# Kernel optimization log

Hardware: AMD Instinct MI355X
Metric: run time of the kernel (lower is better)

## Reference

```python
import jax, jax.numpy as jnp
import numpy as np

B, T, H, NH, L = 2, 2048, 1024, 16, 6
D = H // NH          # head dim = 64
FF = 4 * H           # MLP hidden = 4096
EPS = 1e-5           # torch LayerNorm default

CAUSAL = np.tril(np.ones((T, T), dtype=bool))  # [T,T] lower-triangular mask


def _ln(x, g, b):
    m = jnp.mean(x, axis=-1, keepdims=True)
    v = jnp.mean(jnp.square(x - m), axis=-1, keepdims=True)
    return (x - m) * jax.lax.rsqrt(v + EPS) * g + b


def _block(x, p):
    Wq, bq, Wk, bk, Wv, bv, Wp, bp, W1, b1, W2, b2, g1, be1, g2, be2 = p
    mask = jnp.asarray(CAUSAL)
    # qkv projections -> [B, NH, T, D]
    q = (x @ Wq + bq).reshape(B, T, NH, D).transpose(0, 2, 1, 3)
    k = (x @ Wk + bk).reshape(B, T, NH, D).transpose(0, 2, 1, 3)
    v = (x @ Wv + bv).reshape(B, T, NH, D).transpose(0, 2, 1, 3)
    scores = jnp.einsum('bhtd,bhsd->bhts', q, k) / jnp.sqrt(jnp.float32(D))
    scores = jnp.where(mask, scores, -jnp.inf)
    attn = jax.nn.softmax(scores, axis=-1)
    o = jnp.einsum('bhts,bhsd->bhtd', attn, v)
    o = o.transpose(0, 2, 1, 3).reshape(B, T, H) @ Wp + bp
    x = _ln(x + o, g1, be1)            # residual then ln1 (post-LN, as in source)
    h = jax.nn.gelu(x @ W1 + b1, approximate=False)
    x = _ln(x + h @ W2 + b2, g2, be2)  # residual then ln2
    return x


def setup_inputs() -> dict:
    key = jax.random.key(0)
    ks = jax.random.split(key, 8)
    s = 0.02
    w = lambda k, shape: jax.random.normal(k, shape, jnp.float32) * s
    return {
        'x':  jax.random.normal(ks[0], (B, T, H), jnp.float32),
        'Wq': w(ks[1], (L, H, H)),  'bq': jnp.zeros((L, H), jnp.float32),
        'Wk': w(ks[2], (L, H, H)),  'bk': jnp.zeros((L, H), jnp.float32),
        'Wv': w(ks[3], (L, H, H)),  'bv': jnp.zeros((L, H), jnp.float32),
        'Wp': w(ks[4], (L, H, H)),  'bp': jnp.zeros((L, H), jnp.float32),
        'W1': w(ks[5], (L, H, FF)), 'b1': jnp.zeros((L, FF), jnp.float32),
        'W2': w(ks[6], (L, FF, H)), 'b2': jnp.zeros((L, H), jnp.float32),
        'g1': jnp.ones((L, H), jnp.float32),  'be1': jnp.zeros((L, H), jnp.float32),
        'g2': jnp.ones((L, H), jnp.float32),  'be2': jnp.zeros((L, H), jnp.float32),
    }


def reference(x, Wq, bq, Wk, bk, Wv, bv, Wp, bp, W1, b1, W2, b2, g1, be1, g2, be2):
    params = (Wq, bq, Wk, bk, Wv, bv, Wp, bp, W1, b1, W2, b2, g1, be1, g2, be2)
    y, _ = jax.lax.scan(lambda c, p: (_block(c, p), None), x, params)
    return y
```

## Files before the change

kernel.cpp:

```cpp
#include <hip/hip_runtime.h>

constexpr int cB  = 2;
constexpr int cT  = 2048;
constexpr int cH  = 1024;
constexpr int cNH = 16;
constexpr int cFF = 4096;
constexpr int cL  = 6;
constexpr int cM  = cB * cT;

typedef __attribute__((ext_vector_type(8))) short short8;
typedef __attribute__((ext_vector_type(4))) float f32x4;
typedef __attribute__((ext_vector_type(4))) unsigned short u16x4;
typedef unsigned short u16;

__device__ __forceinline__ u16 f2bf(float f) {
  union { float f; unsigned int u; } v; v.f = f;
  unsigned int u = v.u;
  return (u16)((u + 0x7fffu + ((u >> 16) & 1u)) >> 16);
}

__device__ __forceinline__ void glds16(const void* g, void* l) {
  __builtin_amdgcn_global_load_lds(
      (__attribute__((address_space(1))) void*)(unsigned long long)g,
      (__attribute__((address_space(3))) void*)(unsigned int)(unsigned long long)l,
      16, 0, 0);
}

#define EPI_F32 0
#define EPI_GELU 1
#define EPI_QKV 2

template <int EPI>
__global__ __launch_bounds__(256) void gemm_bt(
    const u16* __restrict__ A,
    const u16* __restrict__ B0, const u16* __restrict__ B1, const u16* __restrict__ B2,
    const float* __restrict__ bias0, const float* __restrict__ bias1, const float* __restrict__ bias2,
    void* __restrict__ out0, void* __restrict__ out1, void* __restrict__ out2, void* __restrict__ out3,
    int M, int N, int K, int ntn)
{
  __shared__ u16 As[128 * 32];
  __shared__ u16 Bs[128 * 32];
  const int tid = threadIdx.x;
  const int wave = tid >> 6;
  const int lane = tid & 63;
  const int l15 = lane & 15;
  const int q4 = lane >> 4;
  const int mt = blockIdx.x;
  const int by = blockIdx.y;
  const int mat = by / ntn;
  const int nt = by - mat * ntn;
  const u16* BT = (mat == 0) ? B0 : ((mat == 1) ? B1 : B2);
  const float* bias = (mat == 0) ? bias0 : ((mat == 1) ? bias1 : bias2);
  void* out = (mat == 0) ? out0 : ((mat == 1) ? out1 : out2);

  const int kz = blockIdx.z;
  const int kpc = K / gridDim.z;
  const int kb0 = kz * kpc, kb1 = kb0 + kpc;
  if (EPI == EPI_F32) {
    void* outs[4] = {out0, out1, out2, out3};
    out = outs[kz];
    if (kz > 0) bias = nullptr;
  }

  const int wr = (wave >> 1) << 6;
  const int wc = (wave & 1) << 6;

  f32x4 acc[4][4] = {};

  const int srow = (wave << 5) + (lane >> 2);
  const int scol = (lane & 3) << 3;
  const u16* Ag = A + (size_t)(mt * 128 + srow) * K + scol;
  const u16* Bg = BT + (size_t)(nt * 128 + srow) * K + scol;
  u16* AsD = As + (wave << 10);
  u16* BsD = Bs + (wave << 10);

  for (int k0 = kb0; k0 < kb1; k0 += 32) {
    glds16(Ag + k0, AsD);
    glds16(Ag + k0 + 16 * K, AsD + 512);
    glds16(Bg + k0, BsD);
    glds16(Bg + k0 + 16 * K, BsD + 512);
    __syncthreads();
    short8 av[4], bv[4];
#pragma unroll
    for (int i = 0; i < 4; ++i)
      av[i] = *(const short8*)(As + ((wr + i * 16 + l15) << 5) + (q4 << 3));
#pragma unroll
    for (int j = 0; j < 4; ++j)
      bv[j] = *(const short8*)(Bs + ((wc + j * 16 + l15) << 5) + (q4 << 3));
#pragma unroll
    for (int i = 0; i < 4; ++i)
#pragma unroll
      for (int j = 0; j < 4; ++j)
        acc[i][j] = __builtin_amdgcn_mfma_f32_16x16x32_bf16(av[i], bv[j], acc[i][j], 0, 0, 0);
    __syncthreads();
  }

  float bj[4];
#pragma unroll
  for (int j = 0; j < 4; ++j) bj[j] = bias ? bias[nt * 128 + wc + j * 16 + l15] : 0.0f;

  const float qscale = (EPI == EPI_QKV && mat == 0) ? 0.125f : 1.0f;

#pragma unroll
  for (int i = 0; i < 4; ++i) {
#pragma unroll
    for (int j = 0; j < 4; ++j) {
      const int n = nt * 128 + wc + j * 16 + l15;
#pragma unroll
      for (int r = 0; r < 4; ++r) {
        const int m = mt * 128 + wr + i * 16 + (q4 << 2) + r;
        float vv = acc[i][j][r] + bj[j];
        if (EPI == EPI_F32) {
          ((float*)out)[(size_t)m * N + n] = vv;
        } else if (EPI == EPI_GELU) {
          float gg = vv * 0.5f * (1.0f + erff(vv * 0.70710678118654752f));
          ((u16*)out)[(size_t)m * N + n] = f2bf(gg);
        } else {
          const int b = m >> 11, t = m & (cT - 1);
          const int h = n >> 6, d = n & 63;
          ((u16*)out)[((((size_t)b * cNH + h) * cT + t) << 6) + d] = f2bf(vv * qscale);
        }
      }
    }
  }
}

__global__ __launch_bounds__(256) void flash_attn(
    const u16* __restrict__ q, const u16* __restrict__ k,
    const u16* __restrict__ v, u16* __restrict__ o)
{
  __shared__ u16 Vt[2][64 * 80];
  __shared__ u16 Pl[8][16 * 80];

  const int tid = threadIdx.x, wave = tid >> 6, lane = tid & 63;
  const int l15 = lane & 15, q4 = lane >> 4;
  const int bx = blockIdx.x;
  const int qtH = 31 - bx;
  const int qtL = bx;
  const int bh = blockIdx.y;
  const u16* qh = q + ((size_t)bh * cT << 6);
  const u16* kh = k + ((size_t)bh * cT << 6);
  const u16* vh = v + ((size_t)bh * cT << 6);

  short8 qfH[2], qfL[2];
#pragma unroll
  for (int kk = 0; kk < 2; ++kk) {
    qfH[kk] = *(const short8*)(qh + (size_t)((qtH << 6) + wave * 16 + l15) * 64 + kk * 32 + q4 * 8);
    qfL[kk] = *(const short8*)(qh + (size_t)((qtL << 6) + wave * 16 + l15) * 64 + kk * 32 + q4 * 8);
  }

  short8 ones;
#pragma unroll
  for (int i = 0; i < 8; ++i) ones[i] = (short)0x3F80;

  uint4 vs0, vs1;
  auto vload = [&](int st) {
    const int s0 = st << 6;
    const u16* src = vh + (size_t)(s0 + lane) * 64 + wave * 8;
    vs0 = *(const uint4*)(src);
    vs1 = *(const uint4*)(src + 32);
  };
  auto vwrite = [&](int buf) {
    u16* Vb = &Vt[buf][0];
    const int s = lane;
#pragma unroll
    for (int rd = 0; rd < 2; ++rd) {
      const int d0 = wave * 8 + rd * 32;
      uint4 vv = rd ? vs1 : vs0;
      Vb[(d0 + 0) * 80 + s] = (u16)(vv.x & 0xffff);
      Vb[(d0 + 1) * 80 + s] = (u16)(vv.x >> 16);
      Vb[(d0 + 2) * 80 + s] = (u16)(vv.y & 0xffff);
      Vb[(d0 + 3) * 80 + s] = (u16)(vv.y >> 16);
      Vb[(d0 + 4) * 80 + s] = (u16)(vv.z & 0xffff);
      Vb[(d0 + 5) * 80 + s] = (u16)(vv.z >> 16);
      Vb[(d0 + 6) * 80 + s] = (u16)(vv.w & 0xffff);
      Vb[(d0 + 7) * 80 + s] = (u16)(vv.w >> 16);
    }
  };

  auto loadK = [&](int st, short8* kf) {
    const int s0 = st << 6;
#pragma unroll
    for (int j = 0; j < 4; ++j)
#pragma unroll
      for (int kk = 0; kk < 2; ++kk)
        kf[j * 2 + kk] = *(const short8*)(kh + (size_t)(s0 + j * 16 + l15) * 64 + kk * 32 + q4 * 8);
  };

  f32x4 oaH[4] = {}, oaL[4] = {};
  f32x4 lsH = {}, lsL = {};

  auto tileQ = [&](int kt, int qt, const short8* qf, const short8* kf,
                   f32x4* oa, f32x4& ls, int buf, u16* pl) {
    f32x4 sa[4];
#pragma unroll
    for (int j = 0; j < 4; ++j) {
      f32x4 zz = {};
      zz = __builtin_amdgcn_mfma_f32_16x16x32_bf16(qf[0], kf[j * 2 + 0], zz, 0, 0, 0);
      zz = __builtin_amdgcn_mfma_f32_16x16x32_bf16(qf[1], kf[j * 2 + 1], zz, 0, 0, 0);
      sa[j] = zz;
    }
    if (kt == qt) {
#pragma unroll
      for (int r = 0; r < 4; ++r) {
        const int trow = wave * 16 + q4 * 4 + r;
#pragma unroll
        for (int j = 0; j < 4; ++j) {
          float pv = (j * 16 + l15 > trow) ? 0.0f : __expf(sa[j][r]);
          pl[(q4 * 4 + r) * 80 + j * 16 + l15] = f2bf(pv);
        }
      }
    } else {
#pragma unroll
      for (int r = 0; r < 4; ++r)
#pragma unroll
        for (int j = 0; j < 4; ++j)
          pl[(q4 * 4 + r) * 80 + j * 16 + l15] = f2bf(__expf(sa[j][r]));
    }
#pragma unroll
    for (int kk = 0; kk < 2; ++kk) {
      short8 pf = *(const short8*)(&pl[l15 * 80 + kk * 32 + q4 * 8]);
      ls = __builtin_amdgcn_mfma_f32_16x16x32_bf16(pf, ones, ls, 0, 0, 0);
#pragma unroll
      for (int jd = 0; jd < 4; ++jd) {
        short8 vf = *(const short8*)(&Vt[buf][(jd * 16 + l15) * 80 + kk * 32 + q4 * 8]);
        oa[jd] = __builtin_amdgcn_mfma_f32_16x16x32_bf16(pf, vf, oa[jd], 0, 0, 0);
      }
    }
  };

  auto tile = [&](int kt, const short8* kf, int buf) {
    tileQ(kt, qtH, qfH, kf, oaH, lsH, buf, &Pl[wave][0]);
    if (kt <= qtL)
      tileQ(kt, qtL, qfL, kf, oaL, lsL, buf, &Pl[wave + 4][0]);
  };

  const int nk = qtH + 1;
  short8 kfA[8], kfB[8];
  vload(0);
  loadK(0, kfA);
  vwrite(0);
  __syncthreads();

  int kt = 0;
  for (; kt + 2 <= nk; kt += 2) {
    vload(kt + 1);
    loadK(kt + 1, kfB);
    tile(kt, kfA, 0);
    vwrite(1);
    __syncthreads();
    if (kt + 2 < nk) { vload(kt + 2); loadK(kt + 2, kfA); }
    tile(kt + 1, kfB, 1);
    if (kt + 2 < nk) vwrite(0);
    __syncthreads();
  }
  if (kt < nk) { tile(kt, kfA, 0); }

  const int b = bh >> 4, h = bh & 15;
#pragma unroll
  for (int r = 0; r < 4; ++r) {
    const int tH = (qtH << 6) + wave * 16 + (q4 << 2) + r;
    const int tL = (qtL << 6) + wave * 16 + (q4 << 2) + r;
    const float invH = 1.0f / lsH[r];
    const float invL = 1.0f / lsL[r];
#pragma unroll
    for (int jd = 0; jd < 4; ++jd) {
      const int d = jd * 16 + l15;
      o[((size_t)(b * cT + tH)) * cH + (h << 6) + d] = f2bf(oaH[jd][r] * invH);
      o[((size_t)(b * cT + tL)) * cH + (h << 6) + d] = f2bf(oaL[jd][r] * invL);
    }
  }
}

template <int NY>
__global__ __launch_bounds__(256) void add_ln_k(
    const float* __restrict__ x,
    const float* __restrict__ y0, const float* __restrict__ y1,
    const float* __restrict__ y2, const float* __restrict__ y3,
    const float* __restrict__ g, const float* __restrict__ be,
    float* __restrict__ xout, u16* __restrict__ xb)
{
  const float* ys[4] = {y0, y1, y2, y3};
  const int row = blockIdx.x;
  const int c = threadIdx.x << 2;
  const size_t base = ((size_t)row << 10) + c;
  f32x4 vv = *(const f32x4*)(x + base);
#pragma unroll
  for (int p = 0; p < NY; ++p) {
    f32x4 yv = *(const f32x4*)(ys[p] + base);
#pragma unroll
    for (int t = 0; t < 4; ++t) vv[t] += yv[t];
  }
  float s1 = vv[0] + vv[1] + vv[2] + vv[3];
  float s2 = vv[0] * vv[0] + vv[1] * vv[1] + vv[2] * vv[2] + vv[3] * vv[3];
#pragma unroll
  for (int off = 1; off < 64; off <<= 1) {
    s1 += __shfl_xor(s1, off);
    s2 += __shfl_xor(s2, off);
  }
  __shared__ float sm[8];
  const int wave = threadIdx.x >> 6, lane = threadIdx.x & 63;
  if (lane == 0) { sm[wave] = s1; sm[wave + 4] = s2; }
  __syncthreads();
  const float S1 = sm[0] + sm[1] + sm[2] + sm[3];
  const float S2 = sm[4] + sm[5] + sm[6] + sm[7];
  const float mean = S1 * (1.0f / cH);
  const float var = S2 * (1.0f / cH) - mean * mean;
  const float rstd = rsqrtf(var + 1e-5f);
  f32x4 gv = *(const f32x4*)(g + c);
  f32x4 bv = *(const f32x4*)(be + c);
  f32x4 ov; u16x4 ob;
#pragma unroll
  for (int t = 0; t < 4; ++t) {
    ov[t] = (vv[t] - mean) * rstd * gv[t] + bv[t];
    ob[t] = f2bf(ov[t]);
  }
  *(f32x4*)(xout + base) = ov;
  *(u16x4*)(xb + base) = ob;
}

__global__ __launch_bounds__(256) void cvt_bf16(const float* __restrict__ in, u16* __restrict__ out)
{
  const size_t i = ((size_t)blockIdx.x * 256 + threadIdx.x) << 2;
  f32x4 vv = *(const f32x4*)(in + i);
  u16x4 ob;
#pragma unroll
  for (int t = 0; t < 4; ++t) ob[t] = f2bf(vv[t]);
  *(u16x4*)(out + i) = ob;
}

struct TransArgs {
  const float* src[6];
  u16* dst[6];
  int Kd[6];
  int Nd[6];
  int tofs[7];
};

__global__ __launch_bounds__(256) void transpose_w(TransArgs ta)
{
  __shared__ float tile[32][33];
  const int bid = blockIdx.x;
  int mi = 0;
#pragma unroll
  for (int i = 0; i < 5; ++i)
    if (bid >= ta.tofs[i + 1]) mi = i + 1;
  const int loc = bid - ta.tofs[mi];
  const int K = ta.Kd[mi], N = ta.Nd[mi];
  const int ntn = N >> 5;
  const int tk = loc / ntn, tn = loc - tk * ntn;
  const int r = threadIdx.x >> 3, c = (threadIdx.x & 7) << 2;
  f32x4 val = *(const f32x4*)(ta.src[mi] + (size_t)(tk * 32 + r) * N + tn * 32 + c);
#pragma unroll
  for (int t = 0; t < 4; ++t) tile[r][c + t] = val[t];
  __syncthreads();
  u16x4 ov;
#pragma unroll
  for (int t = 0; t < 4; ++t) ov[t] = f2bf(tile[c + t][r]);
  *(u16x4*)(ta.dst[mi] + (size_t)(tn * 32 + r) * K + tk * 32 + c) = ov;
}

extern "C" void kernel_launch(void* const* d_in, const int* in_sizes, int n_in,
                              void* d_out, int out_size, void* d_ws, size_t ws_size,
                              hipStream_t stream)
{
  const float* x_in = (const float*)d_in[0];
  const float* Wq = (const float*)d_in[1];
  const float* bq = (const float*)d_in[2];
  const float* Wk = (const float*)d_in[3];
  const float* bk = (const float*)d_in[4];
  const float* Wv = (const float*)d_in[5];
  const float* bv = (const float*)d_in[6];
  const float* Wp = (const float*)d_in[7];
  const float* bp = (const float*)d_in[8];
  const float* W1 = (const float*)d_in[9];
  const float* b1 = (const float*)d_in[10];
  const float* W2 = (const float*)d_in[11];
  const float* b2 = (const float*)d_in[12];
  const float* g1 = (const float*)d_in[13];
  const float* be1 = (const float*)d_in[14];
  const float* g2 = (const float*)d_in[15];
  const float* be2 = (const float*)d_in[16];

  char* w = (char*)d_ws;
  auto alloc = [&](size_t bytes) {
    char* p = w;
    w += (bytes + 255) & ~(size_t)255;
    return (void*)p;
  };
  float* xf = (float*)alloc((size_t)cM * cH * 4);
  u16* xb = (u16*)alloc((size_t)cM * cH * 2);
  u16* qb = (u16*)alloc((size_t)cM * cH * 2);
  u16* kb = (u16*)alloc((size_t)cM * cH * 2);
  u16* vb = (u16*)alloc((size_t)cM * cH * 2);
  u16* ob = (u16*)alloc((size_t)cM * cH * 2);
  u16* hb = (u16*)alloc((size_t)cM * cFF * 2);
  float* yb0 = (float*)alloc((size_t)cM * cH * 4);
  float* yb1 = (float*)alloc((size_t)cM * cH * 4);
  u16* wqT = (u16*)alloc((size_t)cH * cH * 2);
  u16* wkT = (u16*)alloc((size_t)cH * cH * 2);
  u16* wvT = (u16*)alloc((size_t)cH * cH * 2);
  u16* wpT = (u16*)alloc((size_t)cH * cH * 2);
  u16* w1T = (u16*)alloc((size_t)cH * cFF * 2);
  u16* w2T = (u16*)alloc((size_t)cH * cFF * 2);
  float* yb2 = (float*)qb;
  float* yb3 = (float*)vb;

  cvt_bf16<<<cM * cH / 1024, 256, 0, stream>>>(x_in, xb);
  const float* xcur = x_in;

  for (int l = 0; l < cL; ++l) {
    TransArgs ta;
    ta.src[0] = Wq + (size_t)l * cH * cH; ta.dst[0] = wqT; ta.Kd[0] = cH;  ta.Nd[0] = cH;
    ta.src[1] = Wk + (size_t)l * cH * cH; ta.dst[1] = wkT; ta.Kd[1] = cH;  ta.Nd[1] = cH;
    ta.src[2] = Wv + (size_t)l * cH * cH; ta.dst[2] = wvT; ta.Kd[2] = cH;  ta.Nd[2] = cH;
    ta.src[3] = Wp + (size_t)l * cH * cH; ta.dst[3] = wpT; ta.Kd[3] = cH;  ta.Nd[3] = cH;
    ta.src[4] = W1 + (size_t)l * cH * cFF; ta.dst[4] = w1T; ta.Kd[4] = cH;  ta.Nd[4] = cFF;
    ta.src[5] = W2 + (size_t)l * cFF * cH; ta.dst[5] = w2T; ta.Kd[5] = cFF; ta.Nd[5] = cH;
    ta.tofs[0] = 0;    ta.tofs[1] = 1024; ta.tofs[2] = 2048; ta.tofs[3] = 3072;
    ta.tofs[4] = 4096; ta.tofs[5] = 8192; ta.tofs[6] = 12288;
    transpose_w<<<12288, 256, 0, stream>>>(ta);

    gemm_bt<EPI_QKV><<<dim3(32, 24), 256, 0, stream>>>(
        xb, wqT, wkT, wvT, bq + l * cH, bk + l * cH, bv + l * cH,
        qb, kb, vb, nullptr, cM, cH, cH, 8);

    flash_attn<<<dim3(cT / 128, cB * cNH), 256, 0, stream>>>(qb, kb, vb, ob);

    gemm_bt<EPI_F32><<<dim3(32, 8, 2), 256, 0, stream>>>(
        ob, wpT, nullptr, nullptr, bp + l * cH, nullptr, nullptr,
        yb0, yb1, nullptr, nullptr, cM, cH, cH, 8);

    add_ln_k<2><<<cM, 256, 0, stream>>>(xcur, yb0, yb1, nullptr, nullptr,
                                        g1 + l * cH, be1 + l * cH, xf, xb);
    xcur = xf;

    gemm_bt<EPI_GELU><<<dim3(32, 32), 256, 0, stream>>>(
        xb, w1T, nullptr, nullptr, b1 + (size_t)l * cFF, nullptr, nullptr,
        hb, nullptr, nullptr, nullptr, cM, cFF, cH, 32);

    gemm_bt<EPI_F32><<<dim3(32, 8, 4), 256, 0, stream>>>(
        hb, w2T, nullptr, nullptr, b2 + l * cH, nullptr, nullptr,
        yb0, yb1, yb2, yb3, cM, cH, cFF, 8);

    float* xo = (l == cL - 1) ? (float*)d_out : xf;
    add_ln_k<4><<<cM, 256, 0, stream>>>(xcur, yb0, yb1, yb2, yb3,
                                        g2 + l * cH, be2 + l * cH, xo, xb);
  }
}
```

Measured before the change: 2.058 ms.

## Add 256x256-tile, 8-wave GEMM with 4-stage LDS pipeline for QKV and MLP

Adds a new GEMM kernel that uses 256x256 output tiles with 512 threads per block. It streams K in 32-wide chunks through a four-buffer shared-memory ring filled by global_load_lds, and interleaves MFMA bursts with prefetch at raised wave priority. The kernel replaces the 128x128 GEMM for the QKV, MLP-up (GELU) and MLP-down projections, aiming for more data reuse per tile and better latency hiding. The trade-off is far fewer blocks, 192 or 256 per launch on a chip with 256 CUs, and heavy use of shared memory and registers, which can leave CUs underused.

```diff
diff --git a/kernel.cpp b/kernel.cpp
--- a/kernel.cpp
+++ b/kernel.cpp
@@ -29,6 +29,148 @@
 #define EPI_F32 0
 #define EPI_GELU 1
 #define EPI_QKV 2
+
+template <int EPI>
+__global__ __launch_bounds__(512, 2) void gemm256(
+    const u16* __restrict__ A,
+    const u16* __restrict__ B0, const u16* __restrict__ B1, const u16* __restrict__ B2,
+    const float* __restrict__ bias0, const float* __restrict__ bias1, const float* __restrict__ bias2,
+    void* __restrict__ out0, void* __restrict__ out1, void* __restrict__ out2, void* __restrict__ out3,
+    int M, int N, int K, int ntn)
+{
+  __shared__ u16 lds[65536];
+
+  const int tid = threadIdx.x;
+  const int wave = tid >> 6, lane = tid & 63;
+  const int l15 = lane & 15, q4 = lane >> 4;
+  const int wm = wave >> 2, wn = wave & 3;
+  const int mt = blockIdx.x;
+  const int by = blockIdx.y;
+  const int mat = by / ntn;
+  const int nt = by - mat * ntn;
+  const u16* BT = (mat == 0) ? B0 : ((mat == 1) ? B1 : B2);
+  const float* bias = (mat == 0) ? bias0 : ((mat == 1) ? bias1 : bias2);
+  void* out = (mat == 0) ? out0 : ((mat == 1) ? out1 : out2);
+
+  const int kz = blockIdx.z;
+  const int kpc = K / gridDim.z;
+  const int kb0 = kz * kpc;
+  if (EPI == EPI_F32) {
+    void* outs[4] = {out0, out1, out2, out3};
+    out = outs[kz];
+    if (kz > 0) bias = nullptr;
+  }
+  const int nkt = kpc >> 5;
+
+  const u16* Ag[2]; const u16* Bg[2];
+#pragma unroll
+  for (int j = 0; j < 2; ++j) {
+    const int d = j * 8192 + tid * 16;
+    const int l = d ^ (((d >> 6) & 3) << 4);
+    const int srow = l >> 6, skel = (l & 63) >> 1;
+    Ag[j] = A  + (size_t)(mt * 256 + srow) * K + kb0 + skel;
+    Bg[j] = BT + (size_t)(nt * 256 + srow) * K + kb0 + skel;
+  }
+
+  auto stageA = [&](int tt) {
+    u16* dst = lds + ((tt & 3) << 14) + (tid << 3);
+    glds16(Ag[0] + (tt << 5), dst);
+    glds16(Ag[1] + (tt << 5), dst + 4096);
+  };
+  auto stageB = [&](int tt) {
+    u16* dst = lds + ((tt & 3) << 14) + 8192 + (tid << 3);
+    glds16(Bg[0] + (tt << 5), dst);
+    glds16(Bg[1] + (tt << 5), dst + 4096);
+  };
+
+  const int sb = (l15 & 3) << 4;
+
+  f32x4 acc[8][4] = {};
+  short8 a[4], b[4];
+
+  stageA(0); stageB(0); stageA(1); stageB(1);
+  asm volatile("s_waitcnt vmcnt(4)" ::: "memory");
+  __builtin_amdgcn_s_barrier();
+
+  for (int t = 0; t < nkt; ++t) {
+    const u16* As = lds + ((t & 3) << 14);
+    const u16* Bs = As + 8192;
+    const bool pre = (t + 2 < nkt);
+
+#pragma unroll
+    for (int nf = 0; nf < 4; ++nf) {
+      const int r = wn * 64 + nf * 16 + l15;
+      b[nf] = *(const short8*)(Bs + ((((r << 6) + (q4 << 4)) ^ sb) >> 1));
+    }
+#pragma unroll
+    for (int m = 0; m < 4; ++m) {
+      const int r = wm * 128 + m * 16 + l15;
+      a[m] = *(const short8*)(As + ((((r << 6) + (q4 << 4)) ^ sb) >> 1));
+    }
+    if (pre) stageA(t + 2);
+    __builtin_amdgcn_s_barrier();
+    asm volatile("s_waitcnt lgkmcnt(0)" ::: "memory");
+    __builtin_amdgcn_sched_barrier(0);
+    __builtin_amdgcn_s_setprio(1);
+#pragma unroll
+    for (int m = 0; m < 4; ++m)
+#pragma unroll
+      for (int nf = 0; nf < 4; ++nf)
+        acc[m][nf] = __builtin_amdgcn_mfma_f32_16x16x32_bf16(a[m], b[nf], acc[m][nf], 0, 0, 0);
+    __builtin_amdgcn_s_setprio(0);
+    __builtin_amdgcn_s_barrier();
+
+#pragma unroll
+    for (int m = 0; m < 4; ++m) {
+      const int r = wm * 128 + (m + 4) * 16 + l15;
+      a[m] = *(const short8*)(As + ((((r << 6) + (q4 << 4)) ^ sb) >> 1));
+    }
+    if (pre) stageB(t + 2);
+    __builtin_amdgcn_s_barrier();
+    asm volatile("s_waitcnt lgkmcnt(0)" ::: "memory");
+    __builtin_amdgcn_sched_barrier(0);
+    __builtin_amdgcn_s_setprio(1);
+#pragma unroll
+    for (int m = 0; m < 4; ++m)
+#pragma unroll
+      for (int nf = 0; nf < 4; ++nf)
+        acc[m + 4][nf] = __builtin_amdgcn_mfma_f32_16x16x32_bf16(a[m], b[nf], acc[m + 4][nf], 0, 0, 0);
+    __builtin_amdgcn_s_setprio(0);
+    if (pre) asm volatile("s_waitcnt vmcnt(4)" ::: "memory");
+    else     asm volatile("s_waitcnt vmcnt(0)" ::: "memory");
+    __builtin_amdgcn_s_barrier();
+  }
+
+  float bj[4];
+#pragma unroll
+  for (int nf = 0; nf < 4; ++nf)
+    bj[nf] = bias ? bias[nt * 256 + wn * 64 + nf * 16 + l15] : 0.0f;
+
+  const float qscale = (EPI == EPI_QKV && mat == 0) ? 0.125f : 1.0f;
+
+#pragma unroll
+  for (int mf = 0; mf < 8; ++mf) {
+#pragma unroll
+    for (int nf = 0; nf < 4; ++nf) {
+      const int n = nt * 256 + wn * 64 + nf * 16 + l15;
+#pragma unroll
+      for (int r = 0; r < 4; ++r) {
+        const int m = mt * 256 + wm * 128 + mf * 16 + (q4 << 2) + r;
+        float vv = acc[mf][nf][r] + bj[nf];
+        if (EPI == EPI_F32) {
+          ((float*)out)[(size_t)m * N + n] = vv;
+        } else if (EPI == EPI_GELU) {
+          float gg = vv * 0.5f * (1.0f + erff(vv * 0.70710678118654752f));
+          ((u16*)out)[(size_t)m * N + n] = f2bf(gg);
+        } else {
+          const int bb = m >> 11, tt = m & (cT - 1);
+          const int h = n >> 6, d = n & 63;
+          ((u16*)out)[((((size_t)bb * cNH + h) * cT + tt) << 6) + d] = f2bf(vv * qscale);
+        }
+      }
+    }
+  }
+}
 
 template <int EPI>
 __global__ __launch_bounds__(256) void gemm_bt(
@@ -421,9 +563,9 @@
     ta.tofs[4] = 4096; ta.tofs[5] = 8192; ta.tofs[6] = 12288;
     transpose_w<<<12288, 256, 0, stream>>>(ta);
 
-    gemm_bt<EPI_QKV><<<dim3(32, 24), 256, 0, stream>>>(
+    gemm256<EPI_QKV><<<dim3(16, 12), 512, 0, stream>>>(
         xb, wqT, wkT, wvT, bq + l * cH, bk + l * cH, bv + l * cH,
-        qb, kb, vb, nullptr, cM, cH, cH, 8);
+        qb, kb, vb, nullptr, cM, cH, cH, 4);
 
     flash_attn<<<dim3(cT / 128, cB * cNH), 256, 0, stream>>>(qb, kb, vb, ob);
 
@@ -435,13 +577,13 @@
                                         g1 + l * cH, be1 + l * cH, xf, xb);
     xcur = xf;
 
-    gemm_bt<EPI_GELU><<<dim3(32, 32), 256, 0, stream>>>(
+    gemm256<EPI_GELU><<<dim3(16, 16), 512, 0, stream>>>(
         xb, w1T, nullptr, nullptr, b1 + (size_t)l * cFF, nullptr, nullptr,
-        hb, nullptr, nullptr, nullptr, cM, cFF, cH, 32);
-
-    gemm_bt<EPI_F32><<<dim3(32, 8, 4), 256, 0, stream>>>(
+        hb, nullptr, nullptr, nullptr, cM, cFF, cH, 16);
+
+    gemm256<EPI_F32><<<dim3(16, 4, 4), 512, 0, stream>>>(
         hb, w2T, nullptr, nullptr, b2 + l * cH, nullptr, nullptr,
-        yb0, yb1, yb2, yb3, cM, cH, cFF, 8);
+        yb0, yb1, yb2, yb3, cM, cH, cFF, 4);
 
     float* xo = (l == cL - 1) ? (float*)d_out : xf;
     add_ln_k<4><<<cM, 256, 0, stream>>>(xcur, yb0, yb1, yb2, yb3,
```

Result: faster. 1.864 ms (-9.4%).
